# Kernel tuning notes

Measured on AMD Instinct MI355X. Metric: run time of the kernel, lower is better.

Reference implementation:

```python
import jax, jax.numpy as jnp
import numpy as np

N_NODES = 100000
NUM_GRAPHS = 128
FEAT = 128
NUM_CLASSES = 4


def setup_inputs() -> dict:
    key = jax.random.key(0)
    ks = jax.random.split(key, 12)
    x = jax.random.normal(ks[0], (N_NODES, FEAT), dtype=jnp.float32)
    edge_index = jax.random.randint(ks[1], (2, 3200000), 0, N_NODES, dtype=jnp.int64)
    batch = jnp.sort(jax.random.randint(ks[2], (N_NODES,), 0, NUM_GRAPHS, dtype=jnp.int64))

    def glorot(k, fan_in, fan_out):
        lim = float(np.sqrt(6.0 / (fan_in + fan_out)))
        return jax.random.uniform(k, (fan_in, fan_out), jnp.float32, -lim, lim)

    dims = [FEAT, 16, 32, 64, NUM_CLASSES]
    params = {}
    for i in range(4):
        params[f"W{i+1}"] = glorot(ks[3 + i], dims[i], dims[i + 1])
        params[f"b{i+1}"] = jnp.zeros((dims[i + 1],), jnp.float32)
    return dict(x=x, edge_index=edge_index, batch=batch, **params)


def _gcn_norm(edge_index, n):
    # add self-loops, then symmetric normalization deg^{-1/2} A_hat deg^{-1/2}
    loop = jnp.arange(n, dtype=edge_index.dtype)
    row = jnp.concatenate([edge_index[0], loop])  # source
    col = jnp.concatenate([edge_index[1], loop])  # target
    deg = jax.ops.segment_sum(jnp.ones_like(col, jnp.float32), col, num_segments=n)
    dinv = jnp.where(deg > 0, jax.lax.rsqrt(deg), 0.0)
    norm = dinv[row] * dinv[col]  # [E+N]
    return row, col, norm


def _gcn_conv(x, row, col, norm, W, b):
    h = x @ W  # [N, out]
    msg = h[row] * norm[:, None]  # gather + scale, [E+N, out]
    agg = jax.ops.segment_sum(msg, col, num_segments=x.shape[0])
    return agg + b


def reference(x, edge_index, batch, W1, b1, W2, b2, W3, b3, W4, b4):
    n = x.shape[0]
    row, col, norm = _gcn_norm(edge_index, n)
    # dropout is identity in eval mode
    h = jax.nn.relu(_gcn_conv(x, row, col, norm, W1, b1))
    h = jax.nn.relu(_gcn_conv(h, row, col, norm, W2, b2))
    h = jax.nn.relu(_gcn_conv(h, row, col, norm, W3, b3))
    h = _gcn_conv(h, row, col, norm, W4, b4)
    pooled = jax.ops.segment_max(h, batch, num_segments=NUM_GRAPHS)  # [G, C]
    return jax.nn.log_softmax(pooled, axis=1)
```

## Files before the change

### kernel.cpp

```cpp
#include <hip/hip_runtime.h>

#define DIV_UP(a,b) (((a)+(b)-1)/(b))

constexpr int BSHIFT = 7;
constexpr int BNODES = 128;
constexpr int CHUNK_E = 16384;
constexpr int PTH = 512;
constexpr int SCH = 8;
constexpr int SCSH = 14;

__device__ inline unsigned short f2bf(float f) {
    unsigned u = __float_as_uint(f);
    u = u + 0x7FFFu + ((u >> 16) & 1u);
    return (unsigned short)(u >> 16);
}
__device__ inline float bflo(unsigned u) { return __uint_as_float(u << 16); }
__device__ inline float bfhi(unsigned u) { return __uint_as_float(u & 0xFFFF0000u); }

__global__ void zero_int_k(int* p, int n) {
    int i = blockIdx.x * blockDim.x + threadIdx.x;
    if (i < n) p[i] = 0;
}

__global__ void bucket_hist_k(const int* __restrict__ col, int* __restrict__ bhist, int E, int nb) {
    __shared__ int lh[1024];
    for (int i = threadIdx.x; i < 1024; i += blockDim.x) lh[i] = 0;
    __syncthreads();
    int stride = gridDim.x * blockDim.x;
    for (int e = blockIdx.x * blockDim.x + threadIdx.x; e < E; e += stride)
        atomicAdd(&lh[col[e] >> BSHIFT], 1);
    __syncthreads();
    for (int i = threadIdx.x; i < nb; i += blockDim.x) {
        int v = lh[i];
        if (v) atomicAdd(&bhist[i], v);
    }
}

__global__ void bucket_scan_k(const int* __restrict__ bhist, int* __restrict__ bcur, int nb) {
    __shared__ int lds[256];
    int base = threadIdx.x * 4;
    int v[4]; int s = 0;
#pragma unroll
    for (int j = 0; j < 4; j++) { v[j] = (base + j < nb) ? bhist[base + j] : 0; s += v[j]; }
    lds[threadIdx.x] = s; __syncthreads();
    for (int off = 1; off < 256; off <<= 1) {
        int t = (threadIdx.x >= off) ? lds[threadIdx.x - off] : 0;
        __syncthreads();
        lds[threadIdx.x] += t;
        __syncthreads();
    }
    int excl = lds[threadIdx.x] - s;
#pragma unroll
    for (int j = 0; j < 4; j++) {
        if (base + j < nb) bcur[base + j] = excl;
        excl += v[j];
    }
}

__global__ void __launch_bounds__(PTH) partition_k(
        const int* __restrict__ row, const int* __restrict__ col,
        int* __restrict__ bcur, int* __restrict__ part, int E, int nb) {
    __shared__ int lh[1024];
    __shared__ int lbase[1024];
    __shared__ int delta[1024];
    __shared__ unsigned sorted[CHUNK_E];
    __shared__ unsigned short bid[CHUNK_E];
    int tid = threadIdx.x;
    for (int i = tid; i < 1024; i += PTH) lh[i] = 0;
    __syncthreads();
    int base = blockIdx.x * CHUNK_E;
    int end = min(E, base + CHUNK_E);
    for (int e = base + tid; e < end; e += PTH)
        atomicAdd(&lh[col[e] >> BSHIFT], 1);
    __syncthreads();
    int v0 = lh[2 * tid], v1 = lh[2 * tid + 1];
    int s = v0 + v1;
    delta[tid] = s;
    __syncthreads();
    for (int off = 1; off < PTH; off <<= 1) {
        int t = (tid >= off) ? delta[tid - off] : 0;
        __syncthreads();
        delta[tid] += t;
        __syncthreads();
    }
    int excl = delta[tid] - s;
    lbase[2 * tid] = excl;
    lbase[2 * tid + 1] = excl + v0;
    __syncthreads();
    for (int i = tid; i < nb; i += PTH) {
        int c = lh[i];
        int g = c ? atomicAdd(&bcur[i], c) : 0;
        delta[i] = g - lbase[i];
    }
    __syncthreads();
    for (int i = tid; i < nb; i += PTH) lh[i] = lbase[i];
    __syncthreads();
    for (int e = base + tid; e < end; e += PTH) {
        int r = row[e], c = col[e];
        int b = c >> BSHIFT;
        int slot = atomicAdd(&lh[b], 1);
        sorted[slot] = (unsigned)((r << BSHIFT) | (c & (BNODES - 1)));
        bid[slot] = (unsigned short)b;
    }
    __syncthreads();
    int cnt = end - base;
    for (int i = tid; i < cnt; i += PTH) {
        int b = bid[i];
        part[delta[b] + i] = (int)sorted[i];
    }
}

__global__ void __launch_bounds__(256) csr_build_k(
        const int* __restrict__ part, const int* __restrict__ bcur,
        int* __restrict__ cur, float* __restrict__ dinv,
        int* __restrict__ csr, int N) {
    __shared__ int cnt[BNODES * SCH];
    __shared__ int scan_t[256];
    __shared__ int ebounds[2];
    int b = blockIdx.x;
    int tid = threadIdx.x;
    if (tid == 0) { ebounds[0] = b ? bcur[b - 1] : 0; ebounds[1] = bcur[b]; }
    for (int i = tid; i < BNODES * SCH; i += 256) cnt[i] = 0;
    __syncthreads();
    int e0 = ebounds[0], e1 = ebounds[1];
    for (int e = e0 + tid; e < e1; e += 256) {
        unsigned v = (unsigned)part[e];
        int cell = (int)(v & (BNODES - 1)) * SCH + (int)(v >> (BSHIFT + SCSH));
        atomicAdd(&cnt[cell], 1);
    }
    __syncthreads();
    int base4 = tid * 4;
    int c0 = cnt[base4], c1 = cnt[base4+1], c2 = cnt[base4+2], c3 = cnt[base4+3];
    int s = c0 + c1 + c2 + c3;
    scan_t[tid] = s;
    __syncthreads();
    for (int off = 1; off < 256; off <<= 1) {
        int t = (tid >= off) ? scan_t[tid - off] : 0;
        __syncthreads();
        scan_t[tid] += t;
        __syncthreads();
    }
    int excl = scan_t[tid] - s;
    cnt[base4]     = excl;
    cnt[base4 + 1] = excl + c0;
    cnt[base4 + 2] = excl + c0 + c1;
    cnt[base4 + 3] = excl + c0 + c1 + c2;
    __syncthreads();
    if (tid < BNODES) {
        int node = b * BNODES + tid;
        int segstart = cnt[tid * SCH];
        int segend   = (tid == BNODES - 1) ? (e1 - e0) : cnt[(tid + 1) * SCH];
        if (node < N) {
            cur[node]  = e0 + segend;
            dinv[node] = rsqrtf(1.0f + (float)(segend - segstart));
        }
    }
    __syncthreads();
    for (int e = e0 + tid; e < e1; e += 256) {
        unsigned v = (unsigned)part[e];
        int cell = (int)(v & (BNODES - 1)) * SCH + (int)(v >> (BSHIFT + SCSH));
        int p = atomicAdd(&cnt[cell], 1);
        csr[e0 + p] = (int)(v >> BSHIFT);
    }
}

template<int EPI>
__global__ void __launch_bounds__(256) gather16_bf_k(
        const unsigned short* __restrict__ hb, const float* __restrict__ dinv,
        const int* __restrict__ cur, const int* __restrict__ csr,
        const float* __restrict__ b, void* __restrict__ outv, int n) {
    int t2 = blockIdx.x * 256 + threadIdx.x;
    int node = t2 >> 1, t = t2 & 1;
    if (node >= n) return;
    const uint4* hb4 = reinterpret_cast<const uint4*>(hb);
    uint4 sv = hb4[(size_t)node * 2 + t];
    float a0 = bflo(sv.x), a1 = bfhi(sv.x), a2 = bflo(sv.y), a3 = bfhi(sv.y);
    float a4 = bflo(sv.z), a5 = bfhi(sv.z), a6 = bflo(sv.w), a7 = bfhi(sv.w);
    int e0 = node ? cur[node - 1] : 0;
    int e1 = cur[node];
    int e = e0;
    for (; e + 3 < e1; e += 4) {
        int s0 = csr[e], s1 = csr[e+1], s2 = csr[e+2], s3 = csr[e+3];
        uint4 v0 = hb4[(size_t)s0 * 2 + t];
        uint4 v1 = hb4[(size_t)s1 * 2 + t];
        uint4 v2 = hb4[(size_t)s2 * 2 + t];
        uint4 v3 = hb4[(size_t)s3 * 2 + t];
        a0 += (bflo(v0.x) + bflo(v1.x)) + (bflo(v2.x) + bflo(v3.x));
        a1 += (bfhi(v0.x) + bfhi(v1.x)) + (bfhi(v2.x) + bfhi(v3.x));
        a2 += (bflo(v0.y) + bflo(v1.y)) + (bflo(v2.y) + bflo(v3.y));
        a3 += (bfhi(v0.y) + bfhi(v1.y)) + (bfhi(v2.y) + bfhi(v3.y));
        a4 += (bflo(v0.z) + bflo(v1.z)) + (bflo(v2.z) + bflo(v3.z));
        a5 += (bfhi(v0.z) + bfhi(v1.z)) + (bfhi(v2.z) + bfhi(v3.z));
        a6 += (bflo(v0.w) + bflo(v1.w)) + (bflo(v2.w) + bflo(v3.w));
        a7 += (bfhi(v0.w) + bfhi(v1.w)) + (bfhi(v2.w) + bfhi(v3.w));
    }
    for (; e < e1; e++) {
        uint4 v = hb4[(size_t)csr[e] * 2 + t];
        a0 += bflo(v.x); a1 += bfhi(v.x); a2 += bflo(v.y); a3 += bfhi(v.y);
        a4 += bflo(v.z); a5 += bfhi(v.z); a6 += bflo(v.w); a7 += bfhi(v.w);
    }
    float di = dinv[node];
    a0 *= di; a1 *= di; a2 *= di; a3 *= di;
    a4 *= di; a5 *= di; a6 *= di; a7 *= di;
    if constexpr (EPI == 1) {
        int bo = t * 8;
        a0 = fmaxf(a0 + b[bo+0], 0.f) * di; a1 = fmaxf(a1 + b[bo+1], 0.f) * di;
        a2 = fmaxf(a2 + b[bo+2], 0.f) * di; a3 = fmaxf(a3 + b[bo+3], 0.f) * di;
        a4 = fmaxf(a4 + b[bo+4], 0.f) * di; a5 = fmaxf(a5 + b[bo+5], 0.f) * di;
        a6 = fmaxf(a6 + b[bo+6], 0.f) * di; a7 = fmaxf(a7 + b[bo+7], 0.f) * di;
        uint4 pk;
        pk.x = (unsigned)f2bf(a0) | ((unsigned)f2bf(a1) << 16);
        pk.y = (unsigned)f2bf(a2) | ((unsigned)f2bf(a3) << 16);
        pk.z = (unsigned)f2bf(a4) | ((unsigned)f2bf(a5) << 16);
        pk.w = (unsigned)f2bf(a6) | ((unsigned)f2bf(a7) << 16);
        reinterpret_cast<uint4*>(outv)[(size_t)node * 2 + t] = pk;
    } else {
        float* op = (float*)outv + (size_t)node * 16 + t * 8;
        *reinterpret_cast<float4*>(op)     = make_float4(a0, a1, a2, a3);
        *reinterpret_cast<float4*>(op + 4) = make_float4(a4, a5, a6, a7);
    }
}

__global__ void __launch_bounds__(256) gather32_bf_k(
        const unsigned short* __restrict__ hb, const float* __restrict__ dinv,
        const int* __restrict__ cur, const int* __restrict__ csr,
        float* __restrict__ out, int n) {
    int tid4 = blockIdx.x * 256 + threadIdx.x;
    int node = tid4 >> 2, t = tid4 & 3;
    if (node >= n) return;
    const uint4* hb4 = reinterpret_cast<const uint4*>(hb);
    uint4 sv = hb4[(size_t)node * 4 + t];
    float a0 = bflo(sv.x), a1 = bfhi(sv.x), a2 = bflo(sv.y), a3 = bfhi(sv.y);
    float a4 = bflo(sv.z), a5 = bfhi(sv.z), a6 = bflo(sv.w), a7 = bfhi(sv.w);
    int e0 = node ? cur[node - 1] : 0;
    int e1 = cur[node];
    int e = e0;
    for (; e + 3 < e1; e += 4) {
        int s0 = csr[e], s1 = csr[e+1], s2 = csr[e+2], s3 = csr[e+3];
        uint4 v0 = hb4[(size_t)s0 * 4 + t];
        uint4 v1 = hb4[(size_t)s1 * 4 + t];
        uint4 v2 = hb4[(size_t)s2 * 4 + t];
        uint4 v3 = hb4[(size_t)s3 * 4 + t];
        a0 += (bflo(v0.x) + bflo(v1.x)) + (bflo(v2.x) + bflo(v3.x));
        a1 += (bfhi(v0.x) + bfhi(v1.x)) + (bfhi(v2.x) + bfhi(v3.x));
        a2 += (bflo(v0.y) + bflo(v1.y)) + (bflo(v2.y) + bflo(v3.y));
        a3 += (bfhi(v0.y) + bfhi(v1.y)) + (bfhi(v2.y) + bfhi(v3.y));
        a4 += (bflo(v0.z) + bflo(v1.z)) + (bflo(v2.z) + bflo(v3.z));
        a5 += (bfhi(v0.z) + bfhi(v1.z)) + (bfhi(v2.z) + bfhi(v3.z));
        a6 += (bflo(v0.w) + bflo(v1.w)) + (bflo(v2.w) + bflo(v3.w));
        a7 += (bfhi(v0.w) + bfhi(v1.w)) + (bfhi(v2.w) + bfhi(v3.w));
    }
    for (; e < e1; e++) {
        uint4 v = hb4[(size_t)csr[e] * 4 + t];
        a0 += bflo(v.x); a1 += bfhi(v.x); a2 += bflo(v.y); a3 += bfhi(v.y);
        a4 += bflo(v.z); a5 += bfhi(v.z); a6 += bflo(v.w); a7 += bfhi(v.w);
    }
    float di = dinv[node];
    float* op = out + (size_t)node * 32 + t * 8;
    *reinterpret_cast<float4*>(op)     = make_float4(a0*di, a1*di, a2*di, a3*di);
    *reinterpret_cast<float4*>(op + 4) = make_float4(a4*di, a5*di, a6*di, a7*di);
}

__device__ inline unsigned fkey(float x) {
    unsigned u = __float_as_uint(x);
    return (u & 0x80000000u) ? ~u : (u | 0x80000000u);
}
__device__ inline float funkey(unsigned k) {
    unsigned u = (k & 0x80000000u) ? (k & 0x7FFFFFFFu) : ~k;
    return __uint_as_float(u);
}

__global__ void gather4_pool_k(const float* __restrict__ hs, const float* __restrict__ dinv,
                               const int* __restrict__ cur, const int* __restrict__ csr,
                               const float* __restrict__ b4, const int* __restrict__ batch,
                               unsigned* __restrict__ pooled, int n, int num_graphs) {
    __shared__ unsigned lds[128 * 4];
    for (int i = threadIdx.x; i < num_graphs * 4; i += blockDim.x) lds[i] = 0u;
    __syncthreads();
    int node = blockIdx.x * blockDim.x + threadIdx.x;
    if (node < n) {
        float di = dinv[node];
        float4 acc = reinterpret_cast<const float4*>(hs)[node];
        int e0 = node ? cur[node - 1] : 0;
        int e1 = cur[node];
        int e = e0;
        for (; e + 3 < e1; e += 4) {
            int s0 = csr[e], s1 = csr[e+1], s2 = csr[e+2], s3 = csr[e+3];
            float4 v0 = reinterpret_cast<const float4*>(hs)[s0];
            float4 v1 = reinterpret_cast<const float4*>(hs)[s1];
            float4 v2 = reinterpret_cast<const float4*>(hs)[s2];
            float4 v3 = reinterpret_cast<const float4*>(hs)[s3];
            acc.x += (v0.x + v1.x) + (v2.x + v3.x);
            acc.y += (v0.y + v1.y) + (v2.y + v3.y);
            acc.z += (v0.z + v1.z) + (v2.z + v3.z);
            acc.w += (v0.w + v1.w) + (v2.w + v3.w);
        }
        for (; e < e1; e++) {
            float4 v0 = reinterpret_cast<const float4*>(hs)[csr[e]];
            acc.x += v0.x; acc.y += v0.y; acc.z += v0.z; acc.w += v0.w;
        }
        int g = batch[node];
        atomicMax(&lds[g*4+0], fkey(acc.x * di + b4[0]));
        atomicMax(&lds[g*4+1], fkey(acc.y * di + b4[1]));
        atomicMax(&lds[g*4+2], fkey(acc.z * di + b4[2]));
        atomicMax(&lds[g*4+3], fkey(acc.w * di + b4[3]));
    }
    __syncthreads();
    for (int i2 = threadIdx.x; i2 < num_graphs * 4; i2 += blockDim.x) {
        unsigned k = lds[i2];
        if (k) atomicMax(&pooled[i2], k);
    }
}

__global__ void pool_init_k(unsigned* pooled, int total) {
    int i = blockIdx.x * blockDim.x + threadIdx.x;
    if (i < total) pooled[i] = 0u;
}

__global__ void logsoftmax_k(const unsigned* __restrict__ pooled, float* __restrict__ out, int G) {
    int g = blockIdx.x * blockDim.x + threadIdx.x;
    if (g >= G) return;
    float v[4];
#pragma unroll
    for (int j = 0; j < 4; j++) v[j] = funkey(pooled[g*4+j]);
    float m = fmaxf(fmaxf(v[0], v[1]), fmaxf(v[2], v[3]));
    float s = 0.f;
#pragma unroll
    for (int j = 0; j < 4; j++) s += expf(v[j] - m);
    float l = logf(s);
#pragma unroll
    for (int j = 0; j < 4; j++) out[g*4+j] = v[j] - m - l;
}

template<int IN, int OUT, bool RELU, bool BIAS, bool SCALE, bool IBF, bool OBF>
__global__ void __launch_bounds__(256) matmul_k(
        const void* __restrict__ xv, const float* __restrict__ W,
        const float* __restrict__ b, const float* __restrict__ dinv,
        void* __restrict__ yv, int n) {
    constexpr int TN  = 64;
    constexpr int RS  = IN + 4;
    constexpr int OPT = OUT / 4;
    constexpr int NQ  = IN / 4;
    __shared__ float xs[TN * RS];
    __shared__ float Ws[IN * OUT];
    __shared__ float bs[OUT];

    for (int i = threadIdx.x; i < IN * OUT; i += 256) Ws[i] = W[i];
    if (BIAS) for (int i = threadIdx.x; i < OUT; i += 256) bs[i] = b[i];

    int base = blockIdx.x * TN;
    if constexpr (!IBF) {
        const float* x = (const float*)xv;
        for (int i = threadIdx.x; i < TN * NQ; i += 256) {
            int r = i / NQ, c = i % NQ;
            float4 v = make_float4(0.f, 0.f, 0.f, 0.f);
            if (base + r < n) v = reinterpret_cast<const float4*>(x + (size_t)(base + r) * IN)[c];
            *reinterpret_cast<float4*>(&xs[r * RS + c * 4]) = v;
        }
    } else {
        constexpr int NU = IN / 8;
        const uint4* x = (const uint4*)xv;
        for (int i = threadIdx.x; i < TN * NU; i += 256) {
            int r = i / NU, c = i % NU;
            uint4 v = make_uint4(0u, 0u, 0u, 0u);
            if (base + r < n) v = x[(size_t)(base + r) * NU + c];
            float* dst = &xs[r * RS + c * 8];
            dst[0] = bflo(v.x); dst[1] = bfhi(v.x);
            dst[2] = bflo(v.y); dst[3] = bfhi(v.y);
            dst[4] = bflo(v.z); dst[5] = bfhi(v.z);
            dst[6] = bflo(v.w); dst[7] = bfhi(v.w);
        }
    }
    __syncthreads();

    int node = threadIdx.x >> 2;
    int g    = threadIdx.x & 3;
    int j0   = g * OPT;
    int gnode = base + node;
    if (gnode >= n) return;

    float acc[OPT];
#pragma unroll
    for (int jj = 0; jj < OPT; jj++) acc[jj] = 0.f;

    const float* xrow = &xs[node * RS];
#pragma unroll
    for (int k4 = 0; k4 < NQ; k4++) {
        float4 xvv = *reinterpret_cast<const float4*>(&xrow[k4 * 4]);
        float xk[4] = {xvv.x, xvv.y, xvv.z, xvv.w};
#pragma unroll
        for (int kk = 0; kk < 4; kk++) {
            const float* wrow = &Ws[(k4 * 4 + kk) * OUT + j0];
#pragma unroll
            for (int jj = 0; jj < OPT; jj++)
                acc[jj] += xk[kk] * wrow[jj];
        }
    }

    float di = SCALE ? dinv[gnode] : 1.f;
    float vout[OPT];
#pragma unroll
    for (int jj = 0; jj < OPT; jj++) {
        float v = acc[jj] + (BIAS ? bs[j0 + jj] : 0.f);
        if (RELU) v = fmaxf(v, 0.f);
        if (SCALE) v *= di;
        vout[jj] = v;
    }
    if constexpr (OBF) {
        unsigned short* yr = (unsigned short*)yv + (size_t)gnode * OUT + j0;
        if constexpr (OPT % 8 == 0) {
#pragma unroll
            for (int q = 0; q < OPT / 8; q++) {
                uint4 pk;
                pk.x = (unsigned)f2bf(vout[q*8+0]) | ((unsigned)f2bf(vout[q*8+1]) << 16);
                pk.y = (unsigned)f2bf(vout[q*8+2]) | ((unsigned)f2bf(vout[q*8+3]) << 16);
                pk.z = (unsigned)f2bf(vout[q*8+4]) | ((unsigned)f2bf(vout[q*8+5]) << 16);
                pk.w = (unsigned)f2bf(vout[q*8+6]) | ((unsigned)f2bf(vout[q*8+7]) << 16);
                reinterpret_cast<uint4*>(yr)[q] = pk;
            }
        } else {
            uint2 pk;
            pk.x = (unsigned)f2bf(vout[0]) | ((unsigned)f2bf(vout[1]) << 16);
            pk.y = (unsigned)f2bf(vout[2]) | ((unsigned)f2bf(vout[3]) << 16);
            *reinterpret_cast<uint2*>(yr) = pk;
        }
    } else {
        float* yr = (float*)yv + (size_t)gnode * OUT + j0;
        if (OPT % 4 == 0) {
#pragma unroll
            for (int q = 0; q < OPT / 4; q++)
                *reinterpret_cast<float4*>(yr + q * 4) =
                    make_float4(vout[q*4+0], vout[q*4+1], vout[q*4+2], vout[q*4+3]);
        } else {
#pragma unroll
            for (int jj = 0; jj < OPT; jj++) yr[jj] = vout[jj];
        }
    }
}

extern "C" void kernel_launch(void* const* d_in, const int* in_sizes, int n_in,
                              void* d_out, int out_size, void* d_ws, size_t ws_size,
                              hipStream_t stream) {
    const float* x     = (const float*)d_in[0];
    const int*   ei    = (const int*)d_in[1];
    const int*   batch = (const int*)d_in[2];
    const float* W1 = (const float*)d_in[3];
    const float* b1 = (const float*)d_in[4];
    const float* W2 = (const float*)d_in[5];
    const float* b2 = (const float*)d_in[6];
    const float* W3 = (const float*)d_in[7];
    const float* b3 = (const float*)d_in[8];
    const float* W4 = (const float*)d_in[9];
    const float* b4 = (const float*)d_in[10];

    const int N = in_sizes[2];
    const int E = in_sizes[1] / 2;
    const int G = 128;
    const int* row = ei;
    const int* col = ei + E;
    const int NB = DIV_UP(N, BNODES);

    float* ws    = (float*)d_ws;
    float* dinv  = ws;
    int*   cur   = (int*)(dinv + N);
    int*   bhist = cur + N;
    int*   bcur  = bhist + 1024;
    int*   csr   = bcur + 1024;
    float* f16a  = (float*)(csr + E);
    float* f16b  = f16a + (size_t)N * 16;
    float* f32a  = f16b + (size_t)N * 16;
    float* f32b  = f32a + (size_t)N * 32;
    unsigned* pooled = (unsigned*)(f32b + (size_t)N * 32);
    int* part = (int*)f32a;
    unsigned short* hb16a = (unsigned short*)f16a;
    unsigned short* hb16b = (unsigned short*)f16b;
    unsigned short* hb32  = (unsigned short*)f32a;
    unsigned short* hb64  = (unsigned short*)f32a;
    float* f4a = f32b;

    const int B = 256;
    const int gridN = DIV_UP(N, B);
    const int gridM = DIV_UP(N, 64);
    const int grid2 = DIV_UP(2 * N, B);

    zero_int_k<<<DIV_UP(1024, B), B, 0, stream>>>(bhist, 1024);
    bucket_hist_k<<<512, B, 0, stream>>>(col, bhist, E, NB);
    bucket_scan_k<<<1, 256, 0, stream>>>(bhist, bcur, NB);
    partition_k<<<DIV_UP(E, CHUNK_E), PTH, 0, stream>>>(row, col, bcur, part, E, NB);
    csr_build_k<<<NB, 256, 0, stream>>>(part, bcur, cur, dinv, csr, N);

    matmul_k<128,16,false,false,true,false,true><<<gridM, B, 0, stream>>>(x, W1, nullptr, dinv, hb16b, N);
    gather16_bf_k<1><<<grid2, B, 0, stream>>>(hb16b, dinv, cur, csr, b1, hb16a, N);

    gather16_bf_k<0><<<grid2, B, 0, stream>>>(hb16a, dinv, cur, csr, nullptr, f32b, N);
    matmul_k<16,32,true,true,true,false,true><<<gridM, B, 0, stream>>>(f32b, W2, b2, dinv, hb32, N);

    gather32_bf_k<<<DIV_UP(N*4, B), B, 0, stream>>>(hb32, dinv, cur, csr, f32b, N);
    matmul_k<32,64,true,true,true,false,true><<<gridM, B, 0, stream>>>(f32b, W3, b3, dinv, hb64, N);

    matmul_k<64,4,false,false,false,true,false><<<gridM, B, 0, stream>>>(hb64, W4, nullptr, nullptr, f4a, N);
    pool_init_k<<<DIV_UP(G*4, B), B, 0, stream>>>(pooled, G*4);
    gather4_pool_k<<<gridN, B, 0, stream>>>(f4a, dinv, cur, csr, b4, batch, pooled, N, G);

    logsoftmax_k<<<1, 128, 0, stream>>>(pooled, (float*)d_out, G);
}
```

Measured before the change: 242.9 us.

## Fuse layer-2 and layer-3 neighbour gathers with their dense matmuls

Layers 2 and 3 now run the CSR neighbour aggregation in one kernel that stages the aggregated rows in shared memory, then multiplies them by the weight matrix there, adding bias, ReLU and the dinv scale before a bf16 store. This removes the fp32 intermediate written by the separate gather kernels and read back by the matmul kernels, and cuts two launches. In exchange each block loads the weights into LDS and holds a __syncthreads barrier between the irregular gather and the matmul. Buffer aliasing is reassigned so hb64 and f4a do not overlap live data.

```diff
diff --git a/kernel.cpp b/kernel.cpp
--- a/kernel.cpp
+++ b/kernel.cpp
@@ -164,11 +164,10 @@
     }
 }
 
-template<int EPI>
 __global__ void __launch_bounds__(256) gather16_bf_k(
         const unsigned short* __restrict__ hb, const float* __restrict__ dinv,
         const int* __restrict__ cur, const int* __restrict__ csr,
-        const float* __restrict__ b, void* __restrict__ outv, int n) {
+        const float* __restrict__ b, unsigned short* __restrict__ outb, int n) {
     int t2 = blockIdx.x * 256 + threadIdx.x;
     int node = t2 >> 1, t = t2 & 1;
     if (node >= n) return;
@@ -200,65 +199,189 @@
         a4 += bflo(v.z); a5 += bfhi(v.z); a6 += bflo(v.w); a7 += bfhi(v.w);
     }
     float di = dinv[node];
-    a0 *= di; a1 *= di; a2 *= di; a3 *= di;
-    a4 *= di; a5 *= di; a6 *= di; a7 *= di;
-    if constexpr (EPI == 1) {
-        int bo = t * 8;
-        a0 = fmaxf(a0 + b[bo+0], 0.f) * di; a1 = fmaxf(a1 + b[bo+1], 0.f) * di;
-        a2 = fmaxf(a2 + b[bo+2], 0.f) * di; a3 = fmaxf(a3 + b[bo+3], 0.f) * di;
-        a4 = fmaxf(a4 + b[bo+4], 0.f) * di; a5 = fmaxf(a5 + b[bo+5], 0.f) * di;
-        a6 = fmaxf(a6 + b[bo+6], 0.f) * di; a7 = fmaxf(a7 + b[bo+7], 0.f) * di;
-        uint4 pk;
-        pk.x = (unsigned)f2bf(a0) | ((unsigned)f2bf(a1) << 16);
-        pk.y = (unsigned)f2bf(a2) | ((unsigned)f2bf(a3) << 16);
-        pk.z = (unsigned)f2bf(a4) | ((unsigned)f2bf(a5) << 16);
-        pk.w = (unsigned)f2bf(a6) | ((unsigned)f2bf(a7) << 16);
-        reinterpret_cast<uint4*>(outv)[(size_t)node * 2 + t] = pk;
-    } else {
-        float* op = (float*)outv + (size_t)node * 16 + t * 8;
-        *reinterpret_cast<float4*>(op)     = make_float4(a0, a1, a2, a3);
-        *reinterpret_cast<float4*>(op + 4) = make_float4(a4, a5, a6, a7);
-    }
-}
-
-__global__ void __launch_bounds__(256) gather32_bf_k(
+    int bo = t * 8;
+    a0 = fmaxf(a0 * di + b[bo+0], 0.f) * di; a1 = fmaxf(a1 * di + b[bo+1], 0.f) * di;
+    a2 = fmaxf(a2 * di + b[bo+2], 0.f) * di; a3 = fmaxf(a3 * di + b[bo+3], 0.f) * di;
+    a4 = fmaxf(a4 * di + b[bo+4], 0.f) * di; a5 = fmaxf(a5 * di + b[bo+5], 0.f) * di;
+    a6 = fmaxf(a6 * di + b[bo+6], 0.f) * di; a7 = fmaxf(a7 * di + b[bo+7], 0.f) * di;
+    uint4 pk;
+    pk.x = (unsigned)f2bf(a0) | ((unsigned)f2bf(a1) << 16);
+    pk.y = (unsigned)f2bf(a2) | ((unsigned)f2bf(a3) << 16);
+    pk.z = (unsigned)f2bf(a4) | ((unsigned)f2bf(a5) << 16);
+    pk.w = (unsigned)f2bf(a6) | ((unsigned)f2bf(a7) << 16);
+    reinterpret_cast<uint4*>(outb)[(size_t)node * 2 + t] = pk;
+}
+
+__global__ void __launch_bounds__(256) gmm16_32_k(
         const unsigned short* __restrict__ hb, const float* __restrict__ dinv,
         const int* __restrict__ cur, const int* __restrict__ csr,
-        float* __restrict__ out, int n) {
-    int tid4 = blockIdx.x * 256 + threadIdx.x;
-    int node = tid4 >> 2, t = tid4 & 3;
+        const float* __restrict__ W, const float* __restrict__ b,
+        unsigned short* __restrict__ yb, int n) {
+    constexpr int TN = 128, RS = 20;
+    __shared__ float xs[TN * RS];
+    __shared__ float Ws[16 * 32];
+    __shared__ float bs[32];
+    for (int i = threadIdx.x; i < 16 * 32; i += 256) Ws[i] = W[i];
+    if (threadIdx.x < 32) bs[threadIdx.x] = b[threadIdx.x];
+    int base = blockIdx.x * TN;
+    {
+        int nl = threadIdx.x >> 1, t = threadIdx.x & 1;
+        int node = base + nl;
+        if (node < n) {
+            const uint4* hb4 = reinterpret_cast<const uint4*>(hb);
+            uint4 sv = hb4[(size_t)node * 2 + t];
+            float a0 = bflo(sv.x), a1 = bfhi(sv.x), a2 = bflo(sv.y), a3 = bfhi(sv.y);
+            float a4 = bflo(sv.z), a5 = bfhi(sv.z), a6 = bflo(sv.w), a7 = bfhi(sv.w);
+            int e0 = node ? cur[node - 1] : 0;
+            int e1 = cur[node];
+            int e = e0;
+            for (; e + 3 < e1; e += 4) {
+                int s0 = csr[e], s1 = csr[e+1], s2 = csr[e+2], s3 = csr[e+3];
+                uint4 v0 = hb4[(size_t)s0 * 2 + t];
+                uint4 v1 = hb4[(size_t)s1 * 2 + t];
+                uint4 v2 = hb4[(size_t)s2 * 2 + t];
+                uint4 v3 = hb4[(size_t)s3 * 2 + t];
+                a0 += (bflo(v0.x) + bflo(v1.x)) + (bflo(v2.x) + bflo(v3.x));
+                a1 += (bfhi(v0.x) + bfhi(v1.x)) + (bfhi(v2.x) + bfhi(v3.x));
+                a2 += (bflo(v0.y) + bflo(v1.y)) + (bflo(v2.y) + bflo(v3.y));
+                a3 += (bfhi(v0.y) + bfhi(v1.y)) + (bfhi(v2.y) + bfhi(v3.y));
+                a4 += (bflo(v0.z) + bflo(v1.z)) + (bflo(v2.z) + bflo(v3.z));
+                a5 += (bfhi(v0.z) + bfhi(v1.z)) + (bfhi(v2.z) + bfhi(v3.z));
+                a6 += (bflo(v0.w) + bflo(v1.w)) + (bflo(v2.w) + bflo(v3.w));
+                a7 += (bfhi(v0.w) + bfhi(v1.w)) + (bfhi(v2.w) + bfhi(v3.w));
+            }
+            for (; e < e1; e++) {
+                uint4 v = hb4[(size_t)csr[e] * 2 + t];
+                a0 += bflo(v.x); a1 += bfhi(v.x); a2 += bflo(v.y); a3 += bfhi(v.y);
+                a4 += bflo(v.z); a5 += bfhi(v.z); a6 += bflo(v.w); a7 += bfhi(v.w);
+            }
+            float di = dinv[node];
+            float* dst = &xs[nl * RS + t * 8];
+            dst[0] = a0*di; dst[1] = a1*di; dst[2] = a2*di; dst[3] = a3*di;
+            dst[4] = a4*di; dst[5] = a5*di; dst[6] = a6*di; dst[7] = a7*di;
+        }
+    }
+    __syncthreads();
+    int nl = threadIdx.x >> 1, g = threadIdx.x & 1;
+    int node = base + nl;
     if (node >= n) return;
-    const uint4* hb4 = reinterpret_cast<const uint4*>(hb);
-    uint4 sv = hb4[(size_t)node * 4 + t];
-    float a0 = bflo(sv.x), a1 = bfhi(sv.x), a2 = bflo(sv.y), a3 = bfhi(sv.y);
-    float a4 = bflo(sv.z), a5 = bfhi(sv.z), a6 = bflo(sv.w), a7 = bfhi(sv.w);
-    int e0 = node ? cur[node - 1] : 0;
-    int e1 = cur[node];
-    int e = e0;
-    for (; e + 3 < e1; e += 4) {
-        int s0 = csr[e], s1 = csr[e+1], s2 = csr[e+2], s3 = csr[e+3];
-        uint4 v0 = hb4[(size_t)s0 * 4 + t];
-        uint4 v1 = hb4[(size_t)s1 * 4 + t];
-        uint4 v2 = hb4[(size_t)s2 * 4 + t];
-        uint4 v3 = hb4[(size_t)s3 * 4 + t];
-        a0 += (bflo(v0.x) + bflo(v1.x)) + (bflo(v2.x) + bflo(v3.x));
-        a1 += (bfhi(v0.x) + bfhi(v1.x)) + (bfhi(v2.x) + bfhi(v3.x));
-        a2 += (bflo(v0.y) + bflo(v1.y)) + (bflo(v2.y) + bflo(v3.y));
-        a3 += (bfhi(v0.y) + bfhi(v1.y)) + (bfhi(v2.y) + bfhi(v3.y));
-        a4 += (bflo(v0.z) + bflo(v1.z)) + (bflo(v2.z) + bflo(v3.z));
-        a5 += (bfhi(v0.z) + bfhi(v1.z)) + (bfhi(v2.z) + bfhi(v3.z));
-        a6 += (bflo(v0.w) + bflo(v1.w)) + (bflo(v2.w) + bflo(v3.w));
-        a7 += (bfhi(v0.w) + bfhi(v1.w)) + (bfhi(v2.w) + bfhi(v3.w));
-    }
-    for (; e < e1; e++) {
-        uint4 v = hb4[(size_t)csr[e] * 4 + t];
-        a0 += bflo(v.x); a1 += bfhi(v.x); a2 += bflo(v.y); a3 += bfhi(v.y);
-        a4 += bflo(v.z); a5 += bfhi(v.z); a6 += bflo(v.w); a7 += bfhi(v.w);
+    int j0 = g * 16;
+    float acc[16];
+#pragma unroll
+    for (int j = 0; j < 16; j++) acc[j] = 0.f;
+    const float* xrow = &xs[nl * RS];
+#pragma unroll
+    for (int k4 = 0; k4 < 4; k4++) {
+        float4 xv = *reinterpret_cast<const float4*>(&xrow[k4 * 4]);
+        float xk[4] = {xv.x, xv.y, xv.z, xv.w};
+#pragma unroll
+        for (int kk = 0; kk < 4; kk++) {
+            const float* wrow = &Ws[(k4*4+kk) * 32 + j0];
+#pragma unroll
+            for (int j = 0; j < 16; j++) acc[j] += xk[kk] * wrow[j];
+        }
     }
     float di = dinv[node];
-    float* op = out + (size_t)node * 32 + t * 8;
-    *reinterpret_cast<float4*>(op)     = make_float4(a0*di, a1*di, a2*di, a3*di);
-    *reinterpret_cast<float4*>(op + 4) = make_float4(a4*di, a5*di, a6*di, a7*di);
+    unsigned short* yr = yb + (size_t)node * 32 + j0;
+#pragma unroll
+    for (int q = 0; q < 2; q++) {
+        float o[8];
+#pragma unroll
+        for (int j = 0; j < 8; j++)
+            o[j] = fmaxf(acc[q*8+j] + bs[j0 + q*8 + j], 0.f) * di;
+        uint4 pk;
+        pk.x = (unsigned)f2bf(o[0]) | ((unsigned)f2bf(o[1]) << 16);
+        pk.y = (unsigned)f2bf(o[2]) | ((unsigned)f2bf(o[3]) << 16);
+        pk.z = (unsigned)f2bf(o[4]) | ((unsigned)f2bf(o[5]) << 16);
+        pk.w = (unsigned)f2bf(o[6]) | ((unsigned)f2bf(o[7]) << 16);
+        reinterpret_cast<uint4*>(yr)[q] = pk;
+    }
+}
+
+__global__ void __launch_bounds__(256) gmm32_64_k(
+        const unsigned short* __restrict__ hb, const float* __restrict__ dinv,
+        const int* __restrict__ cur, const int* __restrict__ csr,
+        const float* __restrict__ W, const float* __restrict__ b,
+        unsigned short* __restrict__ yb, int n) {
+    constexpr int TN = 64, RS = 36;
+    __shared__ float xs[TN * RS];
+    __shared__ float Ws[32 * 64];
+    __shared__ float bs[64];
+    for (int i = threadIdx.x; i < 32 * 64; i += 256) Ws[i] = W[i];
+    if (threadIdx.x < 64) bs[threadIdx.x] = b[threadIdx.x];
+    int base = blockIdx.x * TN;
+    {
+        int nl = threadIdx.x >> 2, t = threadIdx.x & 3;
+        int node = base + nl;
+        if (node < n) {
+            const uint4* hb4 = reinterpret_cast<const uint4*>(hb);
+            uint4 sv = hb4[(size_t)node * 4 + t];
+            float a0 = bflo(sv.x), a1 = bfhi(sv.x), a2 = bflo(sv.y), a3 = bfhi(sv.y);
+            float a4 = bflo(sv.z), a5 = bfhi(sv.z), a6 = bflo(sv.w), a7 = bfhi(sv.w);
+            int e0 = node ? cur[node - 1] : 0;
+            int e1 = cur[node];
+            int e = e0;
+            for (; e + 3 < e1; e += 4) {
+                int s0 = csr[e], s1 = csr[e+1], s2 = csr[e+2], s3 = csr[e+3];
+                uint4 v0 = hb4[(size_t)s0 * 4 + t];
+                uint4 v1 = hb4[(size_t)s1 * 4 + t];
+                uint4 v2 = hb4[(size_t)s2 * 4 + t];
+                uint4 v3 = hb4[(size_t)s3 * 4 + t];
+                a0 += (bflo(v0.x) + bflo(v1.x)) + (bflo(v2.x) + bflo(v3.x));
+                a1 += (bfhi(v0.x) + bfhi(v1.x)) + (bfhi(v2.x) + bfhi(v3.x));
+                a2 += (bflo(v0.y) + bflo(v1.y)) + (bflo(v2.y) + bflo(v3.y));
+                a3 += (bfhi(v0.y) + bfhi(v1.y)) + (bfhi(v2.y) + bfhi(v3.y));
+                a4 += (bflo(v0.z) + bflo(v1.z)) + (bflo(v2.z) + bflo(v3.z));
+                a5 += (bfhi(v0.z) + bfhi(v1.z)) + (bfhi(v2.z) + bfhi(v3.z));
+                a6 += (bflo(v0.w) + bflo(v1.w)) + (bflo(v2.w) + bflo(v3.w));
+                a7 += (bfhi(v0.w) + bfhi(v1.w)) + (bfhi(v2.w) + bfhi(v3.w));
+            }
+            for (; e < e1; e++) {
+                uint4 v = hb4[(size_t)csr[e] * 4 + t];
+                a0 += bflo(v.x); a1 += bfhi(v.x); a2 += bflo(v.y); a3 += bfhi(v.y);
+                a4 += bflo(v.z); a5 += bfhi(v.z); a6 += bflo(v.w); a7 += bfhi(v.w);
+            }
+            float di = dinv[node];
+            float* dst = &xs[nl * RS + t * 8];
+            dst[0] = a0*di; dst[1] = a1*di; dst[2] = a2*di; dst[3] = a3*di;
+            dst[4] = a4*di; dst[5] = a5*di; dst[6] = a6*di; dst[7] = a7*di;
+        }
+    }
+    __syncthreads();
+    int nl = threadIdx.x >> 2, g = threadIdx.x & 3;
+    int node = base + nl;
+    if (node >= n) return;
+    int j0 = g * 16;
+    float acc[16];
+#pragma unroll
+    for (int j = 0; j < 16; j++) acc[j] = 0.f;
+    const float* xrow = &xs[nl * RS];
+#pragma unroll
+    for (int k4 = 0; k4 < 8; k4++) {
+        float4 xv = *reinterpret_cast<const float4*>(&xrow[k4 * 4]);
+        float xk[4] = {xv.x, xv.y, xv.z, xv.w};
+#pragma unroll
+        for (int kk = 0; kk < 4; kk++) {
+            const float* wrow = &Ws[(k4*4+kk) * 64 + j0];
+#pragma unroll
+            for (int j = 0; j < 16; j++) acc[j] += xk[kk] * wrow[j];
+        }
+    }
+    float di = dinv[node];
+    unsigned short* yr = yb + (size_t)node * 64 + j0;
+#pragma unroll
+    for (int q = 0; q < 2; q++) {
+        float o[8];
+#pragma unroll
+        for (int j = 0; j < 8; j++)
+            o[j] = fmaxf(acc[q*8+j] + bs[j0 + q*8 + j], 0.f) * di;
+        uint4 pk;
+        pk.x = (unsigned)f2bf(o[0]) | ((unsigned)f2bf(o[1]) << 16);
+        pk.y = (unsigned)f2bf(o[2]) | ((unsigned)f2bf(o[3]) << 16);
+        pk.z = (unsigned)f2bf(o[4]) | ((unsigned)f2bf(o[5]) << 16);
+        pk.w = (unsigned)f2bf(o[6]) | ((unsigned)f2bf(o[7]) << 16);
+        reinterpret_cast<uint4*>(yr)[q] = pk;
+    }
 }
 
 __device__ inline unsigned fkey(float x) {
@@ -475,13 +598,14 @@
     unsigned short* hb16a = (unsigned short*)f16a;
     unsigned short* hb16b = (unsigned short*)f16b;
     unsigned short* hb32  = (unsigned short*)f32a;
-    unsigned short* hb64  = (unsigned short*)f32a;
-    float* f4a = f32b;
+    unsigned short* hb64  = (unsigned short*)f32b;
+    float* f4a = f16a;
 
     const int B = 256;
     const int gridN = DIV_UP(N, B);
     const int gridM = DIV_UP(N, 64);
     const int grid2 = DIV_UP(2 * N, B);
+    const int gridF = DIV_UP(N, 128);
 
     zero_int_k<<<DIV_UP(1024, B), B, 0, stream>>>(bhist, 1024);
     bucket_hist_k<<<512, B, 0, stream>>>(col, bhist, E, NB);
@@ -490,13 +614,11 @@
     csr_build_k<<<NB, 256, 0, stream>>>(part, bcur, cur, dinv, csr, N);
 
     matmul_k<128,16,false,false,true,false,true><<<gridM, B, 0, stream>>>(x, W1, nullptr, dinv, hb16b, N);
-    gather16_bf_k<1><<<grid2, B, 0, stream>>>(hb16b, dinv, cur, csr, b1, hb16a, N);
-
-    gather16_bf_k<0><<<grid2, B, 0, stream>>>(hb16a, dinv, cur, csr, nullptr, f32b, N);
-    matmul_k<16,32,true,true,true,false,true><<<gridM, B, 0, stream>>>(f32b, W2, b2, dinv, hb32, N);
-
-    gather32_bf_k<<<DIV_UP(N*4, B), B, 0, stream>>>(hb32, dinv, cur, csr, f32b, N);
-    matmul_k<32,64,true,true,true,false,true><<<gridM, B, 0, stream>>>(f32b, W3, b3, dinv, hb64, N);
+    gather16_bf_k<<<grid2, B, 0, stream>>>(hb16b, dinv, cur, csr, b1, hb16a, N);
+
+    gmm16_32_k<<<gridF, B, 0, stream>>>(hb16a, dinv, cur, csr, W2, b2, hb32, N);
+
+    gmm32_64_k<<<gridM, B, 0, stream>>>(hb32, dinv, cur, csr, W3, b3, hb64, N);
 
     matmul_k<64,4,false,false,false,true,false><<<gridM, B, 0, stream>>>(hb64, W4, nullptr, nullptr, f4a, N);
     pool_init_k<<<DIV_UP(G*4, B), B, 0, stream>>>(pooled, G*4);
```

After: 228.2 us. 6.0% less time.
